# Optimization experiments

Hardware: AMD Instinct MI355X
Metric: run time of the kernel (lower is better)

## Reference

```python
import jax, jax.numpy as jnp
import numpy as np

DIM = 1024
E = 8
N = 4096
HID = 4 * DIM
THRESHOLD = 0.3


def setup_inputs() -> dict:
    key = jax.random.key(0)
    ks = jax.random.split(key, 8)
    s = 0.02
    return {
        "x": jax.random.normal(ks[0], (N, DIM), dtype=jnp.float32),
        "expert_inputs": jax.random.normal(ks[1], (E, N, DIM), dtype=jnp.float32),
        "wg": jax.random.normal(ks[2], (DIM, E), dtype=jnp.float32) * s,
        "bg": jnp.zeros((E,), dtype=jnp.float32),
        "w1": jax.random.normal(ks[3], (E, DIM, HID), dtype=jnp.float32) * s,
        "b1": jnp.zeros((E, HID), dtype=jnp.float32),
        "w2": jax.random.normal(ks[4], (E, HID, DIM), dtype=jnp.float32) * s,
        "b2": jnp.zeros((E, DIM), dtype=jnp.float32),
    }


def reference(x, expert_inputs, wg, bg, w1, b1, w2, b2):
    # Gate: softmax over experts. [N, E]
    gate_scores = jax.nn.softmax(x @ wg + bg, axis=-1)

    # Experts: FeedForward(dim, dim, mult=4) = Linear -> GELU -> Linear, batched over E.
    h = jax.nn.gelu(jnp.einsum('end,edh->enh', expert_inputs, w1) + b1[:, None, :],
                    approximate=False)  # [E, N, HID]
    expert_outputs = jnp.einsum('enh,ehd->end', h, w2) + b2[:, None, :]  # [E, N, D]
    expert_outputs = jnp.transpose(expert_outputs, (1, 0, 2))  # [N, E, D]

    # Threshold mask + renormalized weighted combine.
    mask = gate_scores >= THRESHOLD
    masked_scores = gate_scores * mask.astype(gate_scores.dtype)
    normed = masked_scores / (masked_scores.sum(axis=1, keepdims=True) + 1e-6)
    fused = jnp.einsum('ne,ned->nd', normed, expert_outputs)  # [N, D]

    # Fallback: rows with no expert above threshold take the top-1 expert output.
    top1 = jnp.argmax(gate_scores, axis=1)  # [N]
    fallback = jnp.take_along_axis(expert_outputs, top1[:, None, None], axis=1)[:, 0, :]
    fb_mask = (mask.sum(axis=1) == 0)[:, None]
    fused = jnp.where(fb_mask, fallback, fused)
    return fused, gate_scores
```

## Files before the change

### kernel.cpp

```cpp
#include <hip/hip_runtime.h>
#include <hip/hip_bf16.h>
#include <cstdint>

#define N_TOK 4096
#define DIM_  1024
#define HID_  4096
#define NEXP  8
#define HHALF 2048
#define CAP   (3 * N_TOK)

typedef __attribute__((ext_vector_type(8))) short short8;
typedef __attribute__((ext_vector_type(4))) float f32x4;

__device__ __forceinline__ unsigned short f32_to_bf16(float f) {
    union { float f; uint32_t u; } v;
    v.f = f;
    uint32_t r = (v.u + 0x7fffu + ((v.u >> 16) & 1u)) >> 16;
    return (unsigned short)r;
}

__device__ __forceinline__ float gelu_exact(float x) {
    return 0.5f * x * (1.0f + erff(x * 0.70710678118654752440f));
}

__device__ __forceinline__ void gl_lds16(const unsigned short* g, unsigned short* l) {
    __builtin_amdgcn_global_load_lds(
        (const __attribute__((address_space(1))) void*)g,
        (__attribute__((address_space(3))) void*)l, 16, 0, 0);
}

__global__ __launch_bounds__(256)
void zero_init_kernel(float* __restrict__ fused, int* __restrict__ cnt)
{
    const int b = blockIdx.x;
    if (b < N_TOK) {
        float4* p = (float4*)(fused + (size_t)b * DIM_);
        p[threadIdx.x] = make_float4(0.f, 0.f, 0.f, 0.f);
    } else if (threadIdx.x < NEXP) {
        cnt[threadIdx.x] = 0;
    }
}

__global__ __launch_bounds__(256)
void gate_kernel(const float* __restrict__ x, const float* __restrict__ wg,
                 const float* __restrict__ bg, float* __restrict__ gates,
                 float* __restrict__ wts, int* __restrict__ cnt)
{
    const int wave = threadIdx.x >> 6;
    const int lane = threadIdx.x & 63;
    const int n = blockIdx.x * 4 + wave;
    float acc[NEXP];
#pragma unroll
    for (int e = 0; e < NEXP; e++) acc[e] = 0.0f;
    const float4* xr = (const float4*)(x + (size_t)n * DIM_);
#pragma unroll
    for (int j = 0; j < 4; j++) {
        const int k4 = lane + j * 64;
        const float4 v = xr[k4];
        const float* wr = wg + (size_t)k4 * 4 * NEXP;
#pragma unroll
        for (int e = 0; e < NEXP; e++)
            acc[e] += v.x * wr[e] + v.y * wr[NEXP + e] +
                      v.z * wr[2 * NEXP + e] + v.w * wr[3 * NEXP + e];
    }
#pragma unroll
    for (int e = 0; e < NEXP; e++) {
#pragma unroll
        for (int off = 32; off > 0; off >>= 1)
            acc[e] += __shfl_xor(acc[e], off, 64);
    }
    if (lane == 0) {
        float z[NEXP];
#pragma unroll
        for (int e = 0; e < NEXP; e++) z[e] = acc[e] + bg[e];
        float m = z[0];
#pragma unroll
        for (int e = 1; e < NEXP; e++) m = fmaxf(m, z[e]);
        float p[NEXP], s = 0.0f;
#pragma unroll
        for (int e = 0; e < NEXP; e++) { p[e] = __expf(z[e] - m); s += p[e]; }
        const float invs = 1.0f / s;
        float g[NEXP];
        int top = 0;
#pragma unroll
        for (int e = 0; e < NEXP; e++) {
            g[e] = p[e] * invs;
            gates[(size_t)n * NEXP + e] = g[e];
            if (g[e] > g[top]) top = e;
        }
        float w[NEXP], sm = 0.0f;
        int c = 0;
#pragma unroll
        for (int e = 0; e < NEXP; e++) {
            const bool mk = (g[e] >= 0.3f);
            const float ms = mk ? g[e] : 0.0f;
            sm += ms; c += mk ? 1 : 0;
            w[e] = ms;
        }
        if (c == 0) {
#pragma unroll
            for (int e = 0; e < NEXP; e++) w[e] = 0.0f;
            w[top] = 1.0f;
        } else {
            const float inv = 1.0f / (sm + 1e-6f);
#pragma unroll
            for (int e = 0; e < NEXP; e++) w[e] *= inv;
        }
#pragma unroll
        for (int e = 0; e < NEXP; e++) {
            wts[(size_t)n * NEXP + e] = w[e];
            if (w[e] > 0.0f) atomicAdd(&cnt[e], 1);
        }
    }
}

__global__ void offsets_kernel(const int* __restrict__ cnt, int* __restrict__ off,
                               int* __restrict__ cnt2)
{
    if (threadIdx.x == 0) {
        int a = 0;
        for (int e = 0; e < NEXP; e++) { off[e] = a; a += cnt[e]; cnt2[e] = 0; }
    }
}

__global__ __launch_bounds__(256)
void build_list_kernel(const float* __restrict__ wts, const int* __restrict__ off,
                       int* __restrict__ cnt2, int* __restrict__ gidx,
                       float* __restrict__ wpk)
{
    const int n = blockIdx.x * 256 + threadIdx.x;
    if (n >= N_TOK) return;
#pragma unroll
    for (int e = 0; e < NEXP; e++) {
        const float w = wts[(size_t)n * NEXP + e];
        if (w > 0.0f) {
            const int slot = atomicAdd(&cnt2[e], 1);
            const int g = off[e] + slot;
            gidx[g] = n;
            wpk[g] = w;
        }
    }
}

__global__ __launch_bounds__(256)
void gather_cvt_kernel(const float* __restrict__ ei, const int* __restrict__ cnt,
                       const int* __restrict__ off, const int* __restrict__ gidx,
                       unsigned short* __restrict__ xg)
{
    const int e = blockIdx.y;
    const int ne = cnt[e];
    const int i0 = blockIdx.x * 8;
    if (i0 >= ne) return;
    const int grp = threadIdx.x >> 5;
    const int l32 = threadIdx.x & 31;
    const int i = i0 + grp;
    if (i >= ne) return;
    const int o = off[e];
    const float* src = ei + ((size_t)e * N_TOK + gidx[o + i]) * DIM_;
    unsigned short* dst = xg + (size_t)(o + i) * DIM_;
#pragma unroll
    for (int j = 0; j < 8; j++) {
        const int c = (l32 + j * 32) * 4;
        const float4 v = *(const float4*)(src + c);
        ushort4 u;
        u.x = f32_to_bf16(v.x); u.y = f32_to_bf16(v.y);
        u.z = f32_to_bf16(v.z); u.w = f32_to_bf16(v.w);
        *(ushort4*)(dst + c) = u;
    }
}

__global__ __launch_bounds__(256)
void transpose_cvt3(const float* __restrict__ w1, const float* __restrict__ w2,
                    unsigned short* __restrict__ w1t, unsigned short* __restrict__ w2t)
{
    __shared__ float tile[64][33];
    const int z = blockIdx.y;
    const float* src;
    unsigned short* dst;
    int cb, rb;
    if (z < NEXP) {
        src = w1 + (size_t)z * DIM_ * HID_;
        dst = w1t + (size_t)z * DIM_ * HID_;
        cb = blockIdx.x & 127; rb = blockIdx.x >> 7;
    } else {
        src = w2 + (size_t)(z - NEXP) * HID_ * DIM_;
        dst = w2t + (size_t)(z - NEXP) * HID_ * DIM_;
        cb = blockIdx.x & 31; rb = blockIdx.x >> 5;
    }
    const int C = (z < NEXP) ? HID_ : DIM_;
    const int R = (z < NEXP) ? DIM_ : HID_;
    const int c0 = cb * 32;
    const int r0 = rb * 64;
    const int tx = threadIdx.x & 31;
    const int ty = threadIdx.x >> 5;
#pragma unroll
    for (int i = 0; i < 8; i++)
        tile[ty + i * 8][tx] = src[(size_t)(r0 + ty + i * 8) * C + (c0 + tx)];
    __syncthreads();
#pragma unroll
    for (int i = 0; i < 4; i++) {
        const int c = ty + i * 8;
        ushort2 p;
        p.x = f32_to_bf16(tile[2 * tx][c]);
        p.y = f32_to_bf16(tile[2 * tx + 1][c]);
        *(ushort2*)&dst[(size_t)(c0 + c) * R + r0 + 2 * tx] = p;
    }
}

__global__ __launch_bounds__(256)
void gemm1_k(const unsigned short* __restrict__ xg, const unsigned short* __restrict__ w1t,
             const float* __restrict__ b1, unsigned short* __restrict__ hg,
             const int* __restrict__ cnt, const int* __restrict__ off, int h0)
{
    const int e = blockIdx.z;
    const int ne = cnt[e];
    const int rowBase = blockIdx.y * 64;
    if (rowBase >= ne) return;
    const int o = off[e];
    const int colBase = blockIdx.x * 128;

    __shared__ __align__(16) unsigned short sA[64 * 32];
    __shared__ __align__(16) unsigned short sB[128 * 32];
    const int tid  = threadIdx.x;
    const int lane = tid & 63;
    const int wave = tid >> 6;
    const int wr = wave >> 1, wc = wave & 1;

    f32x4 acc[2][4];
#pragma unroll
    for (int i = 0; i < 2; i++)
#pragma unroll
        for (int j = 0; j < 4; j++)
#pragma unroll
            for (int r = 0; r < 4; r++) acc[i][j][r] = 0.0f;

    const int sr = tid >> 2;
    const int sc = (tid & 3) << 3;
    const int rowA = min(rowBase + sr, ne - 1);
    const unsigned short* ga0 = xg + (size_t)(o + rowA) * DIM_ + sc;
    const unsigned short* gb0 = w1t + ((size_t)e * HID_ + h0 + colBase + sr) * DIM_ + sc;
    const unsigned short* gb1 = gb0 + (size_t)64 * DIM_;
    unsigned short* la0 = sA + tid * 8;
    unsigned short* lb0 = sB + tid * 8;
    unsigned short* lb1 = sB + 2048 + tid * 8;

    const int aoff = (wr * 32 + (lane & 15)) * 32 + ((lane >> 4) << 3);
    const int boff = (wc * 64 + (lane & 15)) * 32 + ((lane >> 4) << 3);

    for (int k0 = 0; k0 < DIM_; k0 += 32) {
        gl_lds16(ga0 + k0, la0);
        gl_lds16(gb0 + k0, lb0);
        gl_lds16(gb1 + k0, lb1);
        __syncthreads();
        short8 av[2], bv[4];
#pragma unroll
        for (int i = 0; i < 2; i++) av[i] = *(const short8*)(sA + aoff + i * 16 * 32);
#pragma unroll
        for (int j = 0; j < 4; j++) bv[j] = *(const short8*)(sB + boff + j * 16 * 32);
#pragma unroll
        for (int i = 0; i < 2; i++)
#pragma unroll
            for (int j = 0; j < 4; j++)
                acc[i][j] = __builtin_amdgcn_mfma_f32_16x16x32_bf16(av[i], bv[j], acc[i][j], 0, 0, 0);
        __syncthreads();
    }

    const int crow = rowBase + wr * 32 + ((lane >> 4) << 2);
    const int ccol = colBase + wc * 64 + (lane & 15);
#pragma unroll
    for (int i = 0; i < 2; i++) {
#pragma unroll
        for (int j = 0; j < 4; j++) {
            const int col = ccol + j * 16;
            const float b = b1[(size_t)e * HID_ + h0 + col];
#pragma unroll
            for (int r = 0; r < 4; r++) {
                const int row = crow + i * 16 + r;
                if (row < ne) {
                    const float v = acc[i][j][r] + b;
                    hg[(size_t)(o + row) * HHALF + col] = f32_to_bf16(gelu_exact(v));
                }
            }
        }
    }
}

__global__ __launch_bounds__(256)
void gemm2_k(const unsigned short* __restrict__ hg, const unsigned short* __restrict__ w2t,
             const float* __restrict__ b2, float* __restrict__ fused,
             const int* __restrict__ cnt, const int* __restrict__ off,
             const int* __restrict__ gidx, const float* __restrict__ wpk, int h0)
{
    const int e = blockIdx.z;
    const int ne = cnt[e];
    const int rowBase = blockIdx.y * 64;
    if (rowBase >= ne) return;
    const int o = off[e];
    const int colBase = (blockIdx.x & 7) * 128;
    const int kc = blockIdx.x >> 3;
    const int kbeg = kc * (HHALF / 2);

    __shared__ __align__(16) unsigned short sA[64 * 32];
    __shared__ __align__(16) unsigned short sB[128 * 32];
    const int tid  = threadIdx.x;
    const int lane = tid & 63;
    const int wave = tid >> 6;
    const int wr = wave >> 1, wc = wave & 1;

    f32x4 acc[2][4];
#pragma unroll
    for (int i = 0; i < 2; i++)
#pragma unroll
        for (int j = 0; j < 4; j++)
#pragma unroll
            for (int r = 0; r < 4; r++) acc[i][j][r] = 0.0f;

    const int sr = tid >> 2;
    const int sc = (tid & 3) << 3;
    const int rowA = min(rowBase + sr, ne - 1);
    const unsigned short* ga0 = hg + (size_t)(o + rowA) * HHALF + kbeg + sc;
    const unsigned short* gb0 = w2t + ((size_t)e * DIM_ + colBase + sr) * HID_ + h0 + kbeg + sc;
    const unsigned short* gb1 = gb0 + (size_t)64 * HID_;
    unsigned short* la0 = sA + tid * 8;
    unsigned short* lb0 = sB + tid * 8;
    unsigned short* lb1 = sB + 2048 + tid * 8;

    const int aoff = (wr * 32 + (lane & 15)) * 32 + ((lane >> 4) << 3);
    const int boff = (wc * 64 + (lane & 15)) * 32 + ((lane >> 4) << 3);

    for (int k0 = 0; k0 < HHALF / 2; k0 += 32) {
        gl_lds16(ga0 + k0, la0);
        gl_lds16(gb0 + k0, lb0);
        gl_lds16(gb1 + k0, lb1);
        __syncthreads();
        short8 av[2], bv[4];
#pragma unroll
        for (int i = 0; i < 2; i++) av[i] = *(const short8*)(sA + aoff + i * 16 * 32);
#pragma unroll
        for (int j = 0; j < 4; j++) bv[j] = *(const short8*)(sB + boff + j * 16 * 32);
#pragma unroll
        for (int i = 0; i < 2; i++)
#pragma unroll
            for (int j = 0; j < 4; j++)
                acc[i][j] = __builtin_amdgcn_mfma_f32_16x16x32_bf16(av[i], bv[j], acc[i][j], 0, 0, 0);
        __syncthreads();
    }

    const int crow = rowBase + wr * 32 + ((lane >> 4) << 2);
    const int ccol = colBase + wc * 64 + (lane & 15);
    const int addBias = (h0 == 0 && kc == 0);
#pragma unroll
    for (int i = 0; i < 2; i++) {
#pragma unroll
        for (int j = 0; j < 4; j++) {
            const int col = ccol + j * 16;
            const float b = addBias ? b2[(size_t)e * DIM_ + col] : 0.0f;
#pragma unroll
            for (int r = 0; r < 4; r++) {
                const int row = crow + i * 16 + r;
                if (row < ne) {
                    const float w = wpk[o + row];
                    const int orow = gidx[o + row];
                    atomicAdd(&fused[(size_t)orow * DIM_ + col], w * (acc[i][j][r] + b));
                }
            }
        }
    }
}

extern "C" void kernel_launch(void* const* d_in, const int* in_sizes, int n_in,
                              void* d_out, int out_size, void* d_ws, size_t ws_size,
                              hipStream_t stream)
{
    const float* x  = (const float*)d_in[0];
    const float* ei = (const float*)d_in[1];
    const float* wg = (const float*)d_in[2];
    const float* bg = (const float*)d_in[3];
    const float* w1 = (const float*)d_in[4];
    const float* b1 = (const float*)d_in[5];
    const float* w2 = (const float*)d_in[6];
    const float* b2 = (const float*)d_in[7];

    float* fused = (float*)d_out;
    float* gates = fused + (size_t)N_TOK * DIM_;

    unsigned short* xg  = (unsigned short*)d_ws;
    unsigned short* hg  = xg  + (size_t)CAP * DIM_;
    unsigned short* w1t = hg  + (size_t)CAP * HHALF;
    unsigned short* w2t = w1t + (size_t)NEXP * HID_ * DIM_;
    float* wts = (float*)(w2t + (size_t)NEXP * DIM_ * HID_);
    float* wpk = wts + (size_t)N_TOK * NEXP;
    int* gidx  = (int*)(wpk + CAP);
    int* cnt   = gidx + CAP;
    int* off   = cnt + NEXP;
    int* cnt2  = off + NEXP;

    zero_init_kernel<<<N_TOK + 1, 256, 0, stream>>>(fused, cnt);
    gate_kernel<<<N_TOK / 4, 256, 0, stream>>>(x, wg, bg, gates, wts, cnt);
    offsets_kernel<<<1, 64, 0, stream>>>(cnt, off, cnt2);
    build_list_kernel<<<N_TOK / 256, 256, 0, stream>>>(wts, off, cnt2, gidx, wpk);

    gather_cvt_kernel<<<dim3(N_TOK / 8, NEXP), 256, 0, stream>>>(ei, cnt, off, gidx, xg);
    transpose_cvt3<<<dim3(2048, 16), 256, 0, stream>>>(w1, w2, w1t, w2t);

    for (int h0 = 0; h0 < HID_; h0 += HHALF) {
        gemm1_k<<<dim3(HHALF / 128, N_TOK / 64, NEXP), 256, 0, stream>>>(
            xg, w1t, b1, hg, cnt, off, h0);
        gemm2_k<<<dim3(16, N_TOK / 64, NEXP), 256, 0, stream>>>(
            hg, w2t, b2, fused, cnt, off, gidx, wpk, h0);
    }
}
```

Before: 672.1 us.

## Enlarge GEMM row tiles to 128 and rewrite weight transpose with swizzled bf16 LDS

Both expert GEMM kernels now compute 128x128 output tiles per block instead of 64x128. Each wave holds a 4x4 set of MFMA accumulators, so every B tile loaded from global memory is reused across twice as many rows, and half as many blocks are launched. The weight transpose-convert kernel now reads float4 vectors into 64x64 tiles, converts them to bf16 before the LDS stage, and uses an XOR-swizzled LDS layout so it can write 16-byte vectors. The larger GEMM tiles raise register use and can waste more work on partially filled tiles for experts with few tokens, and fewer blocks may reduce occupancy.

```diff
diff --git a/kernel.cpp b/kernel.cpp
--- a/kernel.cpp
+++ b/kernel.cpp
@@ -173,37 +173,53 @@
 void transpose_cvt3(const float* __restrict__ w1, const float* __restrict__ w2,
                     unsigned short* __restrict__ w1t, unsigned short* __restrict__ w2t)
 {
-    __shared__ float tile[64][33];
+    __shared__ __align__(16) unsigned short t[64 * 64];
     const int z = blockIdx.y;
     const float* src;
     unsigned short* dst;
-    int cb, rb;
+    int C, R, cb, rb;
     if (z < NEXP) {
         src = w1 + (size_t)z * DIM_ * HID_;
         dst = w1t + (size_t)z * DIM_ * HID_;
-        cb = blockIdx.x & 127; rb = blockIdx.x >> 7;
+        C = HID_; R = DIM_;
+        cb = blockIdx.x & 63; rb = blockIdx.x >> 6;
     } else {
         src = w2 + (size_t)(z - NEXP) * HID_ * DIM_;
         dst = w2t + (size_t)(z - NEXP) * HID_ * DIM_;
-        cb = blockIdx.x & 31; rb = blockIdx.x >> 5;
-    }
-    const int C = (z < NEXP) ? HID_ : DIM_;
-    const int R = (z < NEXP) ? DIM_ : HID_;
-    const int c0 = cb * 32;
-    const int r0 = rb * 64;
-    const int tx = threadIdx.x & 31;
-    const int ty = threadIdx.x >> 5;
-#pragma unroll
-    for (int i = 0; i < 8; i++)
-        tile[ty + i * 8][tx] = src[(size_t)(r0 + ty + i * 8) * C + (c0 + tx)];
+        C = DIM_; R = HID_;
+        cb = blockIdx.x & 15; rb = blockIdx.x >> 4;
+    }
+    const int c0 = cb * 64, r0 = rb * 64;
+    const int tid = threadIdx.x;
+
+    const int rB = (tid >> 4) * 4;
+    const int cB = (tid & 15) * 4;
+    float vv[4][4];
+#pragma unroll
+    for (int p = 0; p < 4; p++) {
+        const float4 v = *(const float4*)(src + (size_t)(r0 + rB + p) * C + c0 + cB);
+        vv[p][0] = v.x; vv[p][1] = v.y; vv[p][2] = v.z; vv[p][3] = v.w;
+    }
+#pragma unroll
+    for (int k = 0; k < 4; k++) {
+        const int c = cB + k;
+        const int s = (c >> 3) & 7;
+        const int addr = c * 64 + (((rB >> 3) ^ s) << 3) + (rB & 7);
+        ushort4 q;
+        q.x = f32_to_bf16(vv[0][k]);
+        q.y = f32_to_bf16(vv[1][k]);
+        q.z = f32_to_bf16(vv[2][k]);
+        q.w = f32_to_bf16(vv[3][k]);
+        *(ushort4*)(t + addr) = q;
+    }
     __syncthreads();
 #pragma unroll
-    for (int i = 0; i < 4; i++) {
-        const int c = ty + i * 8;
-        ushort2 p;
-        p.x = f32_to_bf16(tile[2 * tx][c]);
-        p.y = f32_to_bf16(tile[2 * tx + 1][c]);
-        *(ushort2*)&dst[(size_t)(c0 + c) * R + r0 + 2 * tx] = p;
+    for (int it = 0; it < 2; it++) {
+        const int c = (tid >> 3) + it * 32;
+        const int g = tid & 7;
+        const int s = (c >> 3) & 7;
+        const short8 v8 = *(const short8*)(t + c * 64 + ((g ^ s) << 3));
+        *(short8*)(dst + (size_t)(c0 + c) * R + r0 + g * 8) = v8;
     }
 }
 
@@ -214,21 +230,21 @@
 {
     const int e = blockIdx.z;
     const int ne = cnt[e];
-    const int rowBase = blockIdx.y * 64;
+    const int rowBase = blockIdx.y * 128;
     if (rowBase >= ne) return;
     const int o = off[e];
     const int colBase = blockIdx.x * 128;
 
-    __shared__ __align__(16) unsigned short sA[64 * 32];
+    __shared__ __align__(16) unsigned short sA[128 * 32];
     __shared__ __align__(16) unsigned short sB[128 * 32];
     const int tid  = threadIdx.x;
     const int lane = tid & 63;
     const int wave = tid >> 6;
     const int wr = wave >> 1, wc = wave & 1;
 
-    f32x4 acc[2][4];
-#pragma unroll
-    for (int i = 0; i < 2; i++)
+    f32x4 acc[4][4];
+#pragma unroll
+    for (int i = 0; i < 4; i++)
 #pragma unroll
         for (int j = 0; j < 4; j++)
 #pragma unroll
@@ -236,39 +252,43 @@
 
     const int sr = tid >> 2;
     const int sc = (tid & 3) << 3;
-    const int rowA = min(rowBase + sr, ne - 1);
-    const unsigned short* ga0 = xg + (size_t)(o + rowA) * DIM_ + sc;
+    const int rowA0 = min(rowBase + sr, ne - 1);
+    const int rowA1 = min(rowBase + 64 + sr, ne - 1);
+    const unsigned short* ga0 = xg + (size_t)(o + rowA0) * DIM_ + sc;
+    const unsigned short* ga1 = xg + (size_t)(o + rowA1) * DIM_ + sc;
     const unsigned short* gb0 = w1t + ((size_t)e * HID_ + h0 + colBase + sr) * DIM_ + sc;
     const unsigned short* gb1 = gb0 + (size_t)64 * DIM_;
     unsigned short* la0 = sA + tid * 8;
+    unsigned short* la1 = sA + 2048 + tid * 8;
     unsigned short* lb0 = sB + tid * 8;
     unsigned short* lb1 = sB + 2048 + tid * 8;
 
-    const int aoff = (wr * 32 + (lane & 15)) * 32 + ((lane >> 4) << 3);
+    const int aoff = (wr * 64 + (lane & 15)) * 32 + ((lane >> 4) << 3);
     const int boff = (wc * 64 + (lane & 15)) * 32 + ((lane >> 4) << 3);
 
     for (int k0 = 0; k0 < DIM_; k0 += 32) {
         gl_lds16(ga0 + k0, la0);
+        gl_lds16(ga1 + k0, la1);
         gl_lds16(gb0 + k0, lb0);
         gl_lds16(gb1 + k0, lb1);
         __syncthreads();
-        short8 av[2], bv[4];
-#pragma unroll
-        for (int i = 0; i < 2; i++) av[i] = *(const short8*)(sA + aoff + i * 16 * 32);
+        short8 av[4], bv[4];
+#pragma unroll
+        for (int i = 0; i < 4; i++) av[i] = *(const short8*)(sA + aoff + i * 16 * 32);
 #pragma unroll
         for (int j = 0; j < 4; j++) bv[j] = *(const short8*)(sB + boff + j * 16 * 32);
 #pragma unroll
-        for (int i = 0; i < 2; i++)
+        for (int i = 0; i < 4; i++)
 #pragma unroll
             for (int j = 0; j < 4; j++)
                 acc[i][j] = __builtin_amdgcn_mfma_f32_16x16x32_bf16(av[i], bv[j], acc[i][j], 0, 0, 0);
         __syncthreads();
     }
 
-    const int crow = rowBase + wr * 32 + ((lane >> 4) << 2);
+    const int crow = rowBase + wr * 64 + ((lane >> 4) << 2);
     const int ccol = colBase + wc * 64 + (lane & 15);
 #pragma unroll
-    for (int i = 0; i < 2; i++) {
+    for (int i = 0; i < 4; i++) {
 #pragma unroll
         for (int j = 0; j < 4; j++) {
             const int col = ccol + j * 16;
@@ -293,23 +313,23 @@
 {
     const int e = blockIdx.z;
     const int ne = cnt[e];
-    const int rowBase = blockIdx.y * 64;
+    const int rowBase = blockIdx.y * 128;
     if (rowBase >= ne) return;
     const int o = off[e];
     const int colBase = (blockIdx.x & 7) * 128;
     const int kc = blockIdx.x >> 3;
     const int kbeg = kc * (HHALF / 2);
 
-    __shared__ __align__(16) unsigned short sA[64 * 32];
+    __shared__ __align__(16) unsigned short sA[128 * 32];
     __shared__ __align__(16) unsigned short sB[128 * 32];
     const int tid  = threadIdx.x;
     const int lane = tid & 63;
     const int wave = tid >> 6;
     const int wr = wave >> 1, wc = wave & 1;
 
-    f32x4 acc[2][4];
-#pragma unroll
-    for (int i = 0; i < 2; i++)
+    f32x4 acc[4][4];
+#pragma unroll
+    for (int i = 0; i < 4; i++)
 #pragma unroll
         for (int j = 0; j < 4; j++)
 #pragma unroll
@@ -317,40 +337,44 @@
 
     const int sr = tid >> 2;
     const int sc = (tid & 3) << 3;
-    const int rowA = min(rowBase + sr, ne - 1);
-    const unsigned short* ga0 = hg + (size_t)(o + rowA) * HHALF + kbeg + sc;
+    const int rowA0 = min(rowBase + sr, ne - 1);
+    const int rowA1 = min(rowBase + 64 + sr, ne - 1);
+    const unsigned short* ga0 = hg + (size_t)(o + rowA0) * HHALF + kbeg + sc;
+    const unsigned short* ga1 = hg + (size_t)(o + rowA1) * HHALF + kbeg + sc;
     const unsigned short* gb0 = w2t + ((size_t)e * DIM_ + colBase + sr) * HID_ + h0 + kbeg + sc;
     const unsigned short* gb1 = gb0 + (size_t)64 * HID_;
     unsigned short* la0 = sA + tid * 8;
+    unsigned short* la1 = sA + 2048 + tid * 8;
     unsigned short* lb0 = sB + tid * 8;
     unsigned short* lb1 = sB + 2048 + tid * 8;
 
-    const int aoff = (wr * 32 + (lane & 15)) * 32 + ((lane >> 4) << 3);
+    const int aoff = (wr * 64 + (lane & 15)) * 32 + ((lane >> 4) << 3);
     const int boff = (wc * 64 + (lane & 15)) * 32 + ((lane >> 4) << 3);
 
     for (int k0 = 0; k0 < HHALF / 2; k0 += 32) {
         gl_lds16(ga0 + k0, la0);
+        gl_lds16(ga1 + k0, la1);
         gl_lds16(gb0 + k0, lb0);
         gl_lds16(gb1 + k0, lb1);
         __syncthreads();
-        short8 av[2], bv[4];
-#pragma unroll
-        for (int i = 0; i < 2; i++) av[i] = *(const short8*)(sA + aoff + i * 16 * 32);
+        short8 av[4], bv[4];
+#pragma unroll
+        for (int i = 0; i < 4; i++) av[i] = *(const short8*)(sA + aoff + i * 16 * 32);
 #pragma unroll
         for (int j = 0; j < 4; j++) bv[j] = *(const short8*)(sB + boff + j * 16 * 32);
 #pragma unroll
-        for (int i = 0; i < 2; i++)
+        for (int i = 0; i < 4; i++)
 #pragma unroll
             for (int j = 0; j < 4; j++)
                 acc[i][j] = __builtin_amdgcn_mfma_f32_16x16x32_bf16(av[i], bv[j], acc[i][j], 0, 0, 0);
         __syncthreads();
     }
 
-    const int crow = rowBase + wr * 32 + ((lane >> 4) << 2);
+    const int crow = rowBase + wr * 64 + ((lane >> 4) << 2);
     const int ccol = colBase + wc * 64 + (lane & 15);
     const int addBias = (h0 == 0 && kc == 0);
 #pragma unroll
-    for (int i = 0; i < 2; i++) {
+    for (int i = 0; i < 4; i++) {
 #pragma unroll
         for (int j = 0; j < 4; j++) {
             const int col = ccol + j * 16;
@@ -401,12 +425,12 @@
     build_list_kernel<<<N_TOK / 256, 256, 0, stream>>>(wts, off, cnt2, gidx, wpk);
 
     gather_cvt_kernel<<<dim3(N_TOK / 8, NEXP), 256, 0, stream>>>(ei, cnt, off, gidx, xg);
-    transpose_cvt3<<<dim3(2048, 16), 256, 0, stream>>>(w1, w2, w1t, w2t);
+    transpose_cvt3<<<dim3(1024, 16), 256, 0, stream>>>(w1, w2, w1t, w2t);
 
     for (int h0 = 0; h0 < HID_; h0 += HHALF) {
-        gemm1_k<<<dim3(HHALF / 128, N_TOK / 64, NEXP), 256, 0, stream>>>(
+        gemm1_k<<<dim3(HHALF / 128, N_TOK / 128, NEXP), 256, 0, stream>>>(
             xg, w1t, b1, hg, cnt, off, h0);
-        gemm2_k<<<dim3(16, N_TOK / 64, NEXP), 256, 0, stream>>>(
+        gemm2_k<<<dim3(16, N_TOK / 128, NEXP), 256, 0, stream>>>(
             hg, w2t, b2, fused, cnt, off, gidx, wpk, h0);
     }
 }
```

Result: no change. 677.6 us (+0.8%).
